# Optimization experiments

Measured on AMD Instinct MI355X. Metric: run time of the kernel, lower is better.

## Reference

```python
import jax, jax.numpy as jnp
import numpy as np

T = 4096
D_MODEL = 1024
H = 16          # n_heads
HD = 64         # head_dim = d_model // n_heads
LW = 64         # local_window
LT = 16         # latent_tokens
CHUNK = 32      # remote_chunk_size


def setup_inputs() -> dict:
    key = jax.random.key(0)
    ks = jax.random.split(key, 11)
    s = 0.02
    return {
        "x":  jax.random.normal(ks[0], (T, D_MODEL), dtype=jnp.float32),
        "Wq": jax.random.normal(ks[1], (D_MODEL, D_MODEL), dtype=jnp.float32) * s,
        "bq": jnp.zeros((D_MODEL,), dtype=jnp.float32),
        "Wk": jax.random.normal(ks[2], (D_MODEL, D_MODEL), dtype=jnp.float32) * s,
        "bk": jnp.zeros((D_MODEL,), dtype=jnp.float32),
        "Wv": jax.random.normal(ks[3], (D_MODEL, D_MODEL), dtype=jnp.float32) * s,
        "bv": jnp.zeros((D_MODEL,), dtype=jnp.float32),
        "Wo": jax.random.normal(ks[4], (D_MODEL, D_MODEL), dtype=jnp.float32) * s,
        "bo": jnp.zeros((D_MODEL,), dtype=jnp.float32),
        "Wg": jax.random.normal(ks[5], (H, D_MODEL), dtype=jnp.float32) * s,
        "bg": jnp.zeros((H,), dtype=jnp.float32),
    }


def reference(x, Wq, bq, Wk, bk, Wv, bv, Wo, bo, Wg, bg):
    """Runs prefill: forward_step for each token, returning per-step outputs [T, D_MODEL].

    Local cache = circular FIFO of size LW (append + pop-oldest == ring overwrite;
    softmax is permutation-invariant so slot order is irrelevant).
    Evicted tokens accumulate in pending sums; every CHUNK evictions the mean k/v
    is written into the remote latent ring of size LT (oldest overwritten).
    Attention happens BEFORE appending the current token's k/v, matching the torch code.
    """
    scale = 1.0 / np.sqrt(HD)
    Tn = x.shape[0]
    Q = (x @ Wq.T + bq).reshape(Tn, H, HD)
    K = (x @ Wk.T + bk).reshape(Tn, H, HD)
    V = (x @ Wv.T + bv).reshape(Tn, H, HD)
    G = jax.nn.sigmoid(x @ Wg.T + bg)  # [T, H] simple gate

    z = lambda *s: jnp.zeros(s, dtype=x.dtype)
    init = (z(LW, H, HD), z(LW, H, HD),   # local k/v ring
            z(LT, H, HD), z(LT, H, HD),   # remote k/v ring
            z(H, HD), z(H, HD),           # pending k/v sums
            jnp.int32(0), jnp.int32(0))   # pending count, remote count

    def step(carry, inp):
        lk, lv, rk, rv, pks, pvs, pc, rc = carry
        q, k, v, g, t = inp
        # ---- local attention over filled slots (count = min(t, LW)) ----
        lvalid = jnp.arange(LW) < jnp.minimum(t, LW)
        ls = jnp.einsum('hd,nhd->hn', q, lk) * scale
        ls = jnp.where(lvalid[None, :], ls, -1e30)
        lo = jnp.einsum('hn,nhd->hd', jax.nn.softmax(ls, axis=-1), lv)
        lo = lo * (t > 0)
        # ---- remote (compressed latent) attention ----
        rvalid = jnp.arange(LT) < jnp.minimum(rc, LT)
        rs = jnp.einsum('hd,nhd->hn', q, rk) * scale
        rs = jnp.where(rvalid[None, :], rs, -1e30)
        ro = jnp.einsum('hn,nhd->hd', jax.nn.softmax(rs, axis=-1), rv)
        ro = ro * (rc > 0)
        # ---- gate and combine ----
        gate = g[:, None]
        out = gate * lo + (1.0 - gate) * ro  # [H, HD]
        # ---- append k/v: ring write evicts token t-LW into pending ----
        pos = jnp.mod(t, LW)
        evict = (t >= LW)
        pks = pks + jnp.where(evict, lk[pos], 0.0)
        pvs = pvs + jnp.where(evict, lv[pos], 0.0)
        pc = pc + evict.astype(jnp.int32)
        lk = lk.at[pos].set(k)
        lv = lv.at[pos].set(v)
        # ---- compress pending into remote ring when CHUNK reached ----
        comp = (pc == CHUNK)
        ridx = jnp.mod(rc, LT)
        rk = jnp.where(comp, rk.at[ridx].set(pks / CHUNK), rk)
        rv = jnp.where(comp, rv.at[ridx].set(pvs / CHUNK), rv)
        rc = rc + comp.astype(jnp.int32)
        pks = jnp.where(comp, 0.0, pks)
        pvs = jnp.where(comp, 0.0, pvs)
        pc = jnp.where(comp, 0, pc)
        return (lk, lv, rk, rv, pks, pvs, pc, rc), out

    ts = jnp.arange(Tn, dtype=jnp.int32)
    _, outs = jax.lax.scan(step, init, (Q, K, V, G, ts))
    return outs.reshape(Tn, D_MODEL) @ Wo.T + bo
```

## Files before the change

kernel.cpp:

```cpp
#include <hip/hip_runtime.h>
#include <hip/hip_bf16.h>
#include <math.h>

typedef __attribute__((ext_vector_type(8))) short short8;
typedef __attribute__((ext_vector_type(4))) float f32x4;

#define TT 4096
#define DM 1024
#define NH 16
#define HD 64
#define PSTR 168

typedef __attribute__((address_space(3))) unsigned int lds_u32;
typedef __attribute__((address_space(1))) unsigned int glb_u32;

__device__ __forceinline__ void async_cp16(const void* g, void* l) {
    __builtin_amdgcn_global_load_lds((glb_u32*)g, (lds_u32*)l, 16, 0, 0);
}

__global__ __launch_bounds__(256) void cast_all(
    const float* __restrict__ x,  const float* __restrict__ wq,
    const float* __restrict__ wk, const float* __restrict__ wv,
    const float* __restrict__ wo, const float* __restrict__ wg,
    __hip_bfloat16* __restrict__ xb,  __hip_bfloat16* __restrict__ wqb,
    __hip_bfloat16* __restrict__ wkb, __hip_bfloat16* __restrict__ wvb,
    __hip_bfloat16* __restrict__ wob, __hip_bfloat16* __restrict__ wgb)
{
    int b = blockIdx.x;
    const float* src;
    __hip_bfloat16* dst;
    size_t base;
    if (b < 4096)      { src = x;  dst = xb;  base = (size_t)b * 1024; }
    else if (b < 5120) { src = wq; dst = wqb; base = (size_t)(b - 4096) * 1024; }
    else if (b < 6144) { src = wk; dst = wkb; base = (size_t)(b - 5120) * 1024; }
    else if (b < 7168) { src = wv; dst = wvb; base = (size_t)(b - 6144) * 1024; }
    else if (b < 8192) { src = wo; dst = wob; base = (size_t)(b - 7168) * 1024; }
    else               { src = wg; dst = wgb; base = (size_t)(b - 8192) * 1024; }
    size_t i = base + (size_t)threadIdx.x * 4;
    float4 v = *(const float4*)(src + i);
    __hip_bfloat16 h0 = (__hip_bfloat16)v.x;
    __hip_bfloat16 h1 = (__hip_bfloat16)v.y;
    __hip_bfloat16 h2 = (__hip_bfloat16)v.z;
    __hip_bfloat16 h3 = (__hip_bfloat16)v.w;
    ushort4 u;
    u.x = *(unsigned short*)&h0;
    u.y = *(unsigned short*)&h1;
    u.z = *(unsigned short*)&h2;
    u.w = *(unsigned short*)&h3;
    *(ushort4*)((unsigned short*)dst + i) = u;
}

template <typename OutT>
__global__ __launch_bounds__(256) void gemm128(
    const __hip_bfloat16* __restrict__ A,
    const __hip_bfloat16* __restrict__ B0, const __hip_bfloat16* __restrict__ B1,
    const __hip_bfloat16* __restrict__ B2,
    const float* __restrict__ c0, const float* __restrict__ c1, const float* __restrict__ c2,
    OutT* __restrict__ O0, OutT* __restrict__ O1, OutT* __restrict__ O2)
{
    const int K = DM;
    __shared__ __align__(16) unsigned short sA[128 * 32];
    __shared__ __align__(16) unsigned short sB[128 * 32];

    const int grp = blockIdx.y >> 3;
    const __hip_bfloat16* B = grp == 0 ? B0 : (grp == 1 ? B1 : B2);
    const float* bias       = grp == 0 ? c0 : (grp == 1 ? c1 : c2);
    OutT* O                 = grp == 0 ? O0 : (grp == 1 ? O1 : O2);

    const int tid  = threadIdx.x;
    const int w    = tid >> 6;
    const int lane = tid & 63;
    const int l16  = lane & 15;
    const int quad = lane >> 4;
    const int rowBase = blockIdx.x * 128;
    const int colBase = (blockIdx.y & 7) * 128;

    const int srow   = lane >> 2;
    const int sswz   = (srow & 3) ^ (srow >> 2);
    const int gchunk = (lane & 3) ^ sswz;
    const __hip_bfloat16* gA = A + (size_t)(rowBase + w * 32 + srow) * K + gchunk * 8;
    const __hip_bfloat16* gB = B + (size_t)(colBase + w * 32 + srow) * K + gchunk * 8;
    unsigned short* lA = sA + w * 32 * 32;
    unsigned short* lB = sB + w * 32 * 32;

    const int fswz = (l16 & 3) ^ (l16 >> 2);
    const int mrow = (w & 1) * 64;
    const int ncol = (w >> 1) * 64;

    f32x4 acc[4][4];
#pragma unroll
    for (int i = 0; i < 4; ++i)
#pragma unroll
        for (int j = 0; j < 4; ++j) acc[i][j] = (f32x4){0.f, 0.f, 0.f, 0.f};

    for (int k0 = 0; k0 < K; k0 += 32) {
        __syncthreads();
        async_cp16(gA + k0, lA);
        async_cp16(gA + k0 + (size_t)16 * K, lA + 16 * 32);
        async_cp16(gB + k0, lB);
        async_cp16(gB + k0 + (size_t)16 * K, lB + 16 * 32);
        __syncthreads();

        short8 af[4], bf[4];
#pragma unroll
        for (int mt = 0; mt < 4; ++mt)
            af[mt] = *(const short8*)&sA[(mrow + mt * 16 + l16) * 32 + (quad ^ fswz) * 8];
#pragma unroll
        for (int nt = 0; nt < 4; ++nt)
            bf[nt] = *(const short8*)&sB[(ncol + nt * 16 + l16) * 32 + (quad ^ fswz) * 8];
#pragma unroll
        for (int mt = 0; mt < 4; ++mt)
#pragma unroll
            for (int nt = 0; nt < 4; ++nt)
                acc[mt][nt] = __builtin_amdgcn_mfma_f32_16x16x32_bf16(af[mt], bf[nt], acc[mt][nt], 0, 0, 0);
    }

#pragma unroll
    for (int nt = 0; nt < 4; ++nt) {
        int col = colBase + ncol + nt * 16 + l16;
        float bv = bias[col];
#pragma unroll
        for (int mt = 0; mt < 4; ++mt) {
#pragma unroll
            for (int r = 0; r < 4; ++r) {
                int row = rowBase + mrow + mt * 16 + quad * 4 + r;
                O[(size_t)row * DM + col] = (OutT)(acc[mt][nt][r] + bv);
            }
        }
    }
}

template <typename OutT>
__global__ __launch_bounds__(256) void gemm_n64(
    const __hip_bfloat16* __restrict__ A,
    const __hip_bfloat16* __restrict__ B,
    const float* __restrict__ bias,
    OutT* __restrict__ O)
{
    const int K = DM;
    __shared__ __align__(16) unsigned short sA[128 * 32];
    __shared__ __align__(16) unsigned short sB[64 * 32];

    const int tid  = threadIdx.x;
    const int w    = tid >> 6;
    const int lane = tid & 63;
    const int l16  = lane & 15;
    const int quad = lane >> 4;
    const int rowBase = blockIdx.x * 128;
    const int colBase = blockIdx.y * 64;

    const int srow   = lane >> 2;
    const int sswz   = (srow & 3) ^ (srow >> 2);
    const int gchunk = (lane & 3) ^ sswz;
    const __hip_bfloat16* gA = A + (size_t)(rowBase + w * 32 + srow) * K + gchunk * 8;
    const __hip_bfloat16* gB = B + (size_t)(colBase + w * 16 + srow) * K + gchunk * 8;
    unsigned short* lA = sA + w * 32 * 32;
    unsigned short* lB = sB + w * 16 * 32;

    const int fswz = (l16 & 3) ^ (l16 >> 2);
    const int mrow = w * 32;

    f32x4 acc[2][4];
#pragma unroll
    for (int i = 0; i < 2; ++i)
#pragma unroll
        for (int j = 0; j < 4; ++j) acc[i][j] = (f32x4){0.f, 0.f, 0.f, 0.f};

    for (int k0 = 0; k0 < K; k0 += 32) {
        __syncthreads();
        async_cp16(gA + k0, lA);
        async_cp16(gA + k0 + (size_t)16 * K, lA + 16 * 32);
        async_cp16(gB + k0, lB);
        __syncthreads();

        short8 af[2], bf[4];
#pragma unroll
        for (int mt = 0; mt < 2; ++mt)
            af[mt] = *(const short8*)&sA[(mrow + mt * 16 + l16) * 32 + (quad ^ fswz) * 8];
#pragma unroll
        for (int nt = 0; nt < 4; ++nt)
            bf[nt] = *(const short8*)&sB[(nt * 16 + l16) * 32 + (quad ^ fswz) * 8];
#pragma unroll
        for (int mt = 0; mt < 2; ++mt)
#pragma unroll
            for (int nt = 0; nt < 4; ++nt)
                acc[mt][nt] = __builtin_amdgcn_mfma_f32_16x16x32_bf16(af[mt], bf[nt], acc[mt][nt], 0, 0, 0);
    }

#pragma unroll
    for (int nt = 0; nt < 4; ++nt) {
        int col = colBase + nt * 16 + l16;
        float bv = bias[col];
#pragma unroll
        for (int mt = 0; mt < 2; ++mt) {
#pragma unroll
            for (int r = 0; r < 4; ++r) {
                int row = rowBase + mrow + mt * 16 + quad * 4 + r;
                O[(size_t)row * DM + col] = (OutT)(acc[mt][nt][r] + bv);
            }
        }
    }
}

__global__ __launch_bounds__(64) void g_mfma(
    const __hip_bfloat16* __restrict__ xb,
    const __hip_bfloat16* __restrict__ Wgb,
    const float* __restrict__ bg,
    float* __restrict__ G)
{
    const int lane = threadIdx.x;
    const int l16  = lane & 15;
    const int quad = lane >> 4;
    const int t0   = blockIdx.x * 16;
    const __hip_bfloat16* ap = xb + (size_t)(t0 + l16) * DM + quad * 8;
    const __hip_bfloat16* bp = Wgb + (size_t)l16 * DM + quad * 8;
    f32x4 acc = (f32x4){0.f, 0.f, 0.f, 0.f};
#pragma unroll 4
    for (int k0 = 0; k0 < DM; k0 += 32) {
        short8 a = *(const short8*)(ap + k0);
        short8 b = *(const short8*)(bp + k0);
        acc = __builtin_amdgcn_mfma_f32_16x16x32_bf16(a, b, acc, 0, 0, 0);
    }
    float bgv = bg[l16];
#pragma unroll
    for (int r = 0; r < 4; ++r) {
        int t = t0 + quad * 4 + r;
        float z = acc[r] + bgv;
        G[t * NH + l16] = 1.f / (1.f + __expf(-z));
    }
}

__global__ __launch_bounds__(256) void chunk_kernel(
    const __hip_bfloat16* __restrict__ K,
    const __hip_bfloat16* __restrict__ V,
    __hip_bfloat16* __restrict__ CK,
    __hip_bfloat16* __restrict__ CV)
{
    const int c = blockIdx.x;
    const int d = blockIdx.y * 256 + threadIdx.x;
    float ak = 0.f, av = 0.f;
    for (int i = 0; i < 32; ++i) {
        ak += (float)K[(size_t)(c * 32 + i) * DM + d];
        av += (float)V[(size_t)(c * 32 + i) * DM + d];
    }
    CK[(size_t)c * DM + d] = (__hip_bfloat16)(ak * (1.f / 32.f));
    CV[(size_t)c * DM + d] = (__hip_bfloat16)(av * (1.f / 32.f));
}

__global__ __launch_bounds__(256) void attn_mfma(
    const __hip_bfloat16* __restrict__ Q,
    const __hip_bfloat16* __restrict__ K,
    const __hip_bfloat16* __restrict__ V,
    const __hip_bfloat16* __restrict__ CK,
    const __hip_bfloat16* __restrict__ CV,
    const float* __restrict__ G,
    __hip_bfloat16* __restrict__ Aout)
{
    __shared__ alignas(16) unsigned short Pls[64 * PSTR];
    __shared__ alignas(16) unsigned short Vts[64 * PSTR];

    const int h   = blockIdx.y;
    const int t0  = blockIdx.x * 64;
    const int tid = threadIdx.x;
    const int w    = tid >> 6;
    const int lane = tid & 63;
    const int l16  = lane & 15;
    const int quad = lane >> 4;
    const float scale = 0.125f;

    const int rc0  = (t0 >= 96) ? ((t0 - 64) >> 5) : 0;
    const int cmin = rc0 > 16 ? rc0 - 16 : 0;

    const unsigned short* Vu  = (const unsigned short*)V;
    const unsigned short* CVu = (const unsigned short*)CV;

    {
#pragma unroll
        for (int gg = 0; gg < 2; ++gg) {
            const int g = w * 2 + gg;
#pragma unroll
            for (int i = 0; i < 2; ++i) {
                const int pair = lane + 64 * i;
                if (pair < 80) {
                    const int j = pair * 2;
                    const unsigned short *s0, *s1;
                    if (j < 128) {
                        int tok0 = t0 - 64 + j; if (tok0 < 0) tok0 = 0;
                        int tok1 = t0 - 63 + j; if (tok1 < 0) tok1 = 0;
                        s0 = Vu + (size_t)tok0 * DM + h * 64 + g * 8;
                        s1 = Vu + (size_t)tok1 * DM + h * 64 + g * 8;
                    } else {
                        int c0 = cmin + (j - 128); if (c0 > 127) c0 = 127;
                        int c1 = c0 + 1;           if (c1 > 127) c1 = 127;
                        s0 = CVu + (size_t)c0 * DM + h * 64 + g * 8;
                        s1 = CVu + (size_t)c1 * DM + h * 64 + g * 8;
                    }
                    short8 v0 = *(const short8*)s0;
                    short8 v1 = *(const short8*)s1;
#pragma unroll
                    for (int e = 0; e < 8; ++e) {
                        ushort2 pk;
                        pk.x = (unsigned short)v0[e];
                        pk.y = (unsigned short)v1[e];
                        *(ushort2*)&Vts[(g * 8 + e) * PSTR + j] = pk;
                    }
                }
            }
        }
    }

    const __hip_bfloat16* qp = Q + (size_t)(t0 + w * 16 + l16) * DM + h * 64 + quad * 8;
    short8 qf0 = *(const short8*)(qp);
    short8 qf1 = *(const short8*)(qp + 32);

    f32x4 sc[8];
#pragma unroll
    for (int jt = 0; jt < 8; ++jt) {
        int j = jt * 16 + l16;
        int tok = t0 - 64 + j;
        tok = tok < 0 ? 0 : tok;
        const __hip_bfloat16* kp = K + (size_t)tok * DM + h * 64 + quad * 8;
        short8 b0 = *(const short8*)(kp);
        short8 b1 = *(const short8*)(kp + 32);
        f32x4 a = __builtin_amdgcn_mfma_f32_16x16x32_bf16(qf0, b0, (f32x4){0.f,0.f,0.f,0.f}, 0, 0, 0);
        sc[jt]  = __builtin_amdgcn_mfma_f32_16x16x32_bf16(qf1, b1, a, 0, 0, 0);
    }
    f32x4 sc2[2];
#pragma unroll
    for (int jt = 0; jt < 2; ++jt) {
        int c = cmin + jt * 16 + l16;
        if (c > 127) c = 127;
        const __hip_bfloat16* cp = CK + (size_t)c * DM + h * 64 + quad * 8;
        short8 b0 = *(const short8*)(cp);
        short8 b1 = *(const short8*)(cp + 32);
        f32x4 a = __builtin_amdgcn_mfma_f32_16x16x32_bf16(qf0, b0, (f32x4){0.f,0.f,0.f,0.f}, 0, 0, 0);
        sc2[jt] = __builtin_amdgcn_mfma_f32_16x16x32_bf16(qf1, b1, a, 0, 0, 0);
    }

    __syncthreads();

    const int rbase = w * 16 + quad * 4;
    float gl[4], g2[4];
    float mx[4], sm[4], mx2[4], sm2[4];
#pragma unroll
    for (int reg = 0; reg < 4; ++reg) {
        int rr = rbase + reg;
        int t  = t0 + rr;
        float g = G[t * NH + h];
        int rc = (t >= 96) ? ((t - 64) >> 5) : 0;
        gl[reg] = (t > 0)  ? g        : 0.f;
        g2[reg] = (rc > 0) ? (1.f - g) : 0.f;

        int jlo = rr > (64 - t0) ? rr : (64 - t0);
        int jhi = rr + 63;
        float m = -1e30f;
#pragma unroll
        for (int jt = 0; jt < 8; ++jt) {
            int j = jt * 16 + l16;
            float s = (j >= jlo && j <= jhi) ? sc[jt][reg] * scale : -1e30f;
            sc[jt][reg] = s;
            m = fmaxf(m, s);
        }
        mx[reg] = m;

        int nvis = rc < 16 ? rc : 16;
        int clo = rc - nvis, chi = rc - 1;
        float m2 = -1e30f;
#pragma unroll
        for (int jt = 0; jt < 2; ++jt) {
            int c = cmin + jt * 16 + l16;
            float s = (c >= clo && c <= chi) ? sc2[jt][reg] * scale : -1e30f;
            sc2[jt][reg] = s;
            m2 = fmaxf(m2, s);
        }
        mx2[reg] = m2;
    }
#pragma unroll
    for (int off = 1; off <= 8; off <<= 1)
#pragma unroll
        for (int reg = 0; reg < 4; ++reg) {
            mx[reg]  = fmaxf(mx[reg],  __shfl_xor(mx[reg],  off));
            mx2[reg] = fmaxf(mx2[reg], __shfl_xor(mx2[reg], off));
        }
#pragma unroll
    for (int reg = 0; reg < 4; ++reg) {
        float s = 0.f, s2 = 0.f;
#pragma unroll
        for (int jt = 0; jt < 8; ++jt) {
            float p = __expf(sc[jt][reg] - mx[reg]);
            sc[jt][reg] = p;
            s += p;
        }
#pragma unroll
        for (int jt = 0; jt < 2; ++jt) {
            float p = __expf(sc2[jt][reg] - mx2[reg]);
            sc2[jt][reg] = p;
            s2 += p;
        }
        sm[reg] = s; sm2[reg] = s2;
    }
#pragma unroll
    for (int off = 1; off <= 8; off <<= 1)
#pragma unroll
        for (int reg = 0; reg < 4; ++reg) {
            sm[reg]  += __shfl_xor(sm[reg],  off);
            sm2[reg] += __shfl_xor(sm2[reg], off);
        }

#pragma unroll
    for (int reg = 0; reg < 4; ++reg) {
        float f1 = gl[reg] / sm[reg];
        float f2 = g2[reg] / sm2[reg];
        int rowoff = (rbase + reg) * PSTR;
#pragma unroll
        for (int jt = 0; jt < 8; ++jt) {
            __hip_bfloat16 hb = (__hip_bfloat16)(sc[jt][reg] * f1);
            Pls[rowoff + jt * 16 + l16] = *(unsigned short*)&hb;
        }
#pragma unroll
        for (int jt = 0; jt < 2; ++jt) {
            __hip_bfloat16 hb = (__hip_bfloat16)(sc2[jt][reg] * f2);
            Pls[rowoff + 128 + jt * 16 + l16] = *(unsigned short*)&hb;
        }
    }
    asm volatile("s_waitcnt lgkmcnt(0)" ::: "memory");

    f32x4 o[4];
#pragma unroll
    for (int nt = 0; nt < 4; ++nt) o[nt] = (f32x4){0.f, 0.f, 0.f, 0.f};
#pragma unroll
    for (int kt = 0; kt < 5; ++kt) {
        short8 a = *(const short8*)&Pls[(w * 16 + l16) * PSTR + kt * 32 + quad * 8];
#pragma unroll
        for (int nt = 0; nt < 4; ++nt) {
            int dd = nt * 16 + l16;
            short8 b = *(const short8*)&Vts[dd * PSTR + kt * 32 + quad * 8];
            o[nt] = __builtin_amdgcn_mfma_f32_16x16x32_bf16(a, b, o[nt], 0, 0, 0);
        }
    }

#pragma unroll
    for (int nt = 0; nt < 4; ++nt) {
#pragma unroll
        for (int reg = 0; reg < 4; ++reg) {
            int row = t0 + rbase + reg;
            int col = h * 64 + nt * 16 + l16;
            Aout[(size_t)row * DM + col] = (__hip_bfloat16)(o[nt][reg]);
        }
    }
}

extern "C" void kernel_launch(void* const* d_in, const int* in_sizes, int n_in,
                              void* d_out, int out_size, void* d_ws, size_t ws_size,
                              hipStream_t stream)
{
    const float* x  = (const float*)d_in[0];
    const float* Wq = (const float*)d_in[1];
    const float* bq = (const float*)d_in[2];
    const float* Wk = (const float*)d_in[3];
    const float* bk = (const float*)d_in[4];
    const float* Wv = (const float*)d_in[5];
    const float* bv = (const float*)d_in[6];
    const float* Wo = (const float*)d_in[7];
    const float* bo = (const float*)d_in[8];
    const float* Wg = (const float*)d_in[9];
    const float* bg = (const float*)d_in[10];
    float* out = (float*)d_out;

    char* ws = (char*)d_ws;
    const size_t MB = 1024 * 1024;
    __hip_bfloat16* xb  = (__hip_bfloat16*)(ws + 0 * MB);
    __hip_bfloat16* Qb  = (__hip_bfloat16*)(ws + 8 * MB);
    __hip_bfloat16* Kb  = (__hip_bfloat16*)(ws + 16 * MB);
    __hip_bfloat16* Vb  = (__hip_bfloat16*)(ws + 24 * MB);
    __hip_bfloat16* Ab  = (__hip_bfloat16*)(ws + 32 * MB);
    __hip_bfloat16* Wqb = (__hip_bfloat16*)(ws + 40 * MB);
    __hip_bfloat16* Wkb = (__hip_bfloat16*)(ws + 42 * MB);
    __hip_bfloat16* Wvb = (__hip_bfloat16*)(ws + 44 * MB);
    __hip_bfloat16* Wob = (__hip_bfloat16*)(ws + 46 * MB);
    __hip_bfloat16* CKb = (__hip_bfloat16*)(ws + 48 * MB);
    __hip_bfloat16* CVb = (__hip_bfloat16*)(ws + 48 * MB + 256*1024);
    float* Gf           = (float*)(ws + 48 * MB + 512 * 1024);
    __hip_bfloat16* Wgb = (__hip_bfloat16*)(ws + 48 * MB + 768*1024);

    cast_all<<<dim3(8208), 256, 0, stream>>>(x, Wq, Wk, Wv, Wo, Wg,
                                             xb, Wqb, Wkb, Wvb, Wob, Wgb);

    gemm128<__hip_bfloat16><<<dim3(32, 24), 256, 0, stream>>>(
        xb, Wqb, Wkb, Wvb, bq, bk, bv, Qb, Kb, Vb);
    g_mfma<<<dim3(256), 64, 0, stream>>>(xb, Wgb, bg, Gf);
    chunk_kernel<<<dim3(128, 4), 256, 0, stream>>>(Kb, Vb, CKb, CVb);
    attn_mfma<<<dim3(64, 16), 256, 0, stream>>>(Qb, Kb, Vb, CKb, CVb, Gf, Ab);
    gemm_n64<float><<<dim3(32, 16), 256, 0, stream>>>(Ab, Wob, bo, out);
}
```

Baseline: 177.3 us.

## Fuse gate projection and chunk-mean compression into the QKV GEMM kernel

```diff
diff --git a/kernel.cpp b/kernel.cpp
--- a/kernel.cpp
+++ b/kernel.cpp
@@ -56,13 +56,45 @@
     const __hip_bfloat16* __restrict__ B0, const __hip_bfloat16* __restrict__ B1,
     const __hip_bfloat16* __restrict__ B2,
     const float* __restrict__ c0, const float* __restrict__ c1, const float* __restrict__ c2,
-    OutT* __restrict__ O0, OutT* __restrict__ O1, OutT* __restrict__ O2)
+    OutT* __restrict__ O0, OutT* __restrict__ O1, OutT* __restrict__ O2,
+    const __hip_bfloat16* __restrict__ Wg, const float* __restrict__ bgp,
+    float* __restrict__ Gf,
+    __hip_bfloat16* __restrict__ CK, __hip_bfloat16* __restrict__ CV)
 {
     const int K = DM;
+    const int grp = blockIdx.y >> 3;
+
+    if (grp == 3) {
+        const int lane = threadIdx.x & 63;
+        const int w    = threadIdx.x >> 6;
+        const int l16  = lane & 15;
+        const int quad = lane >> 4;
+#pragma unroll
+        for (int u = 0; u < 2; ++u) {
+            const int t0 = blockIdx.x * 128 + w * 32 + u * 16;
+            const __hip_bfloat16* ap = A  + (size_t)(t0 + l16) * DM + quad * 8;
+            const __hip_bfloat16* bp = Wg + (size_t)l16 * DM + quad * 8;
+            f32x4 acc = (f32x4){0.f, 0.f, 0.f, 0.f};
+#pragma unroll 4
+            for (int k0 = 0; k0 < DM; k0 += 32) {
+                short8 a = *(const short8*)(ap + k0);
+                short8 b = *(const short8*)(bp + k0);
+                acc = __builtin_amdgcn_mfma_f32_16x16x32_bf16(a, b, acc, 0, 0, 0);
+            }
+            float bgv = bgp[l16];
+#pragma unroll
+            for (int r = 0; r < 4; ++r) {
+                int t = t0 + quad * 4 + r;
+                float z = acc[r] + bgv;
+                Gf[t * NH + l16] = 1.f / (1.f + __expf(-z));
+            }
+        }
+        return;
+    }
+
     __shared__ __align__(16) unsigned short sA[128 * 32];
     __shared__ __align__(16) unsigned short sB[128 * 32];
 
-    const int grp = blockIdx.y >> 3;
     const __hip_bfloat16* B = grp == 0 ? B0 : (grp == 1 ? B1 : B2);
     const float* bias       = grp == 0 ? c0 : (grp == 1 ? c1 : c2);
     OutT* O                 = grp == 0 ? O0 : (grp == 1 ? O1 : O2);
@@ -119,12 +151,25 @@
     for (int nt = 0; nt < 4; ++nt) {
         int col = colBase + ncol + nt * 16 + l16;
         float bv = bias[col];
+        float cs0 = 0.f, cs1 = 0.f;
 #pragma unroll
         for (int mt = 0; mt < 4; ++mt) {
 #pragma unroll
             for (int r = 0; r < 4; ++r) {
                 int row = rowBase + mrow + mt * 16 + quad * 4 + r;
-                O[(size_t)row * DM + col] = (OutT)(acc[mt][nt][r] + bv);
+                float v = acc[mt][nt][r] + bv;
+                O[(size_t)row * DM + col] = (OutT)v;
+                if (mt < 2) cs0 += v; else cs1 += v;
+            }
+        }
+        if (grp >= 1) {
+            cs0 += __shfl_xor(cs0, 16); cs0 += __shfl_xor(cs0, 32);
+            cs1 += __shfl_xor(cs1, 16); cs1 += __shfl_xor(cs1, 32);
+            if (quad == 0) {
+                __hip_bfloat16* C = (grp == 1) ? CK : CV;
+                int cbase = blockIdx.x * 4 + (w & 1) * 2;
+                C[(size_t)cbase * DM + col]       = (__hip_bfloat16)(cs0 * (1.f / 32.f));
+                C[(size_t)(cbase + 1) * DM + col] = (__hip_bfloat16)(cs1 * (1.f / 32.f));
             }
         }
     }
@@ -200,51 +245,6 @@
             }
         }
     }
-}
-
-__global__ __launch_bounds__(64) void g_mfma(
-    const __hip_bfloat16* __restrict__ xb,
-    const __hip_bfloat16* __restrict__ Wgb,
-    const float* __restrict__ bg,
-    float* __restrict__ G)
-{
-    const int lane = threadIdx.x;
-    const int l16  = lane & 15;
-    const int quad = lane >> 4;
-    const int t0   = blockIdx.x * 16;
-    const __hip_bfloat16* ap = xb + (size_t)(t0 + l16) * DM + quad * 8;
-    const __hip_bfloat16* bp = Wgb + (size_t)l16 * DM + quad * 8;
-    f32x4 acc = (f32x4){0.f, 0.f, 0.f, 0.f};
-#pragma unroll 4
-    for (int k0 = 0; k0 < DM; k0 += 32) {
-        short8 a = *(const short8*)(ap + k0);
-        short8 b = *(const short8*)(bp + k0);
-        acc = __builtin_amdgcn_mfma_f32_16x16x32_bf16(a, b, acc, 0, 0, 0);
-    }
-    float bgv = bg[l16];
-#pragma unroll
-    for (int r = 0; r < 4; ++r) {
-        int t = t0 + quad * 4 + r;
-        float z = acc[r] + bgv;
-        G[t * NH + l16] = 1.f / (1.f + __expf(-z));
-    }
-}
-
-__global__ __launch_bounds__(256) void chunk_kernel(
-    const __hip_bfloat16* __restrict__ K,
-    const __hip_bfloat16* __restrict__ V,
-    __hip_bfloat16* __restrict__ CK,
-    __hip_bfloat16* __restrict__ CV)
-{
-    const int c = blockIdx.x;
-    const int d = blockIdx.y * 256 + threadIdx.x;
-    float ak = 0.f, av = 0.f;
-    for (int i = 0; i < 32; ++i) {
-        ak += (float)K[(size_t)(c * 32 + i) * DM + d];
-        av += (float)V[(size_t)(c * 32 + i) * DM + d];
-    }
-    CK[(size_t)c * DM + d] = (__hip_bfloat16)(ak * (1.f / 32.f));
-    CV[(size_t)c * DM + d] = (__hip_bfloat16)(av * (1.f / 32.f));
 }
 
 __global__ __launch_bounds__(256) void attn_mfma(
@@ -486,10 +486,9 @@
     cast_all<<<dim3(8208), 256, 0, stream>>>(x, Wq, Wk, Wv, Wo, Wg,
                                              xb, Wqb, Wkb, Wvb, Wob, Wgb);
 
-    gemm128<__hip_bfloat16><<<dim3(32, 24), 256, 0, stream>>>(
-        xb, Wqb, Wkb, Wvb, bq, bk, bv, Qb, Kb, Vb);
-    g_mfma<<<dim3(256), 64, 0, stream>>>(xb, Wgb, bg, Gf);
-    chunk_kernel<<<dim3(128, 4), 256, 0, stream>>>(Kb, Vb, CKb, CVb);
+    gemm128<__hip_bfloat16><<<dim3(32, 25), 256, 0, stream>>>(
+        xb, Wqb, Wkb, Wvb, bq, bk, bv, Qb, Kb, Vb,
+        Wgb, bg, Gf, CKb, CVb);
     attn_mfma<<<dim3(64, 16), 256, 0, stream>>>(Qb, Kb, Vb, CKb, CVb, Gf, Ab);
     gemm_n64<float><<<dim3(32, 16), 256, 0, stream>>>(Ab, Wob, bo, out);
 }
```

Result: slower. 185.1 us (+4.4%).
